# Performance work log

Measured on AMD Instinct MI355X. Metric: run time of the kernel, lower is better.

The kernel has to match this reference:

```python
import jax, jax.numpy as jnp
import numpy as np

N = 50000   # nodes
E = 800000  # edges (avg degree 16)
H = 128     # hidden_dim / emb_dim
OUT = 128   # out_dim
NUM_BOND_TYPE = 6
NUM_BOND_DIR = 6


def setup_inputs() -> dict:
    key = jax.random.key(0)
    ks = jax.random.split(key, 12)
    s = 0.05
    return {
        "x": jax.random.normal(ks[0], (N, H), jnp.float32),
        "edge_index": jax.random.randint(ks[1], (2, E), 0, N),
        "edge_attr": jax.random.randint(ks[2], (E, 2), 0, 6),
        "prelu_a": jnp.float32(0.25),  # PReLU single shared slope (torch default)
        "W_enc": jax.random.normal(ks[3], (H, H), jnp.float32) * s,  # enc_to_dec, no bias
        "edge_emb1": jax.random.normal(ks[4], (NUM_BOND_TYPE, H), jnp.float32) * s,
        "edge_emb2": jax.random.normal(ks[5], (NUM_BOND_DIR, H), jnp.float32) * s,
        "W1": jax.random.normal(ks[6], (H, 2 * H), jnp.float32) * s,
        "b1": jnp.zeros((2 * H,), jnp.float32),
        "W2": jax.random.normal(ks[7], (2 * H, OUT), jnp.float32) * s,
        "b2": jnp.zeros((OUT,), jnp.float32),
    }


def reference(x, edge_index, edge_attr, prelu_a, W_enc, edge_emb1, edge_emb2, W1, b1, W2, b2):
    n = x.shape[0]
    # GNNDecoder: PReLU then enc_to_dec linear (no bias)
    x = jnp.where(x > 0, x, prelu_a * x)
    x = x @ W_enc

    # GINConv.forward: add self loops, self-loop edge_attr = [5, 0]
    loop = jnp.arange(n)
    src = jnp.concatenate([edge_index[0], loop])  # [E+N]
    dst = jnp.concatenate([edge_index[1], loop])  # [E+N]
    ea1 = jnp.concatenate([edge_attr[:, 0], jnp.full((n,), 5, edge_attr.dtype)])
    ea2 = jnp.concatenate([edge_attr[:, 1], jnp.zeros((n,), edge_attr.dtype)])

    # edge embedding lookup + gather-add message + scatter-add aggregate
    edge_emb = edge_emb1[ea1] + edge_emb2[ea2]          # [E+N, H]
    msg = x[src] + edge_emb                             # message(x_j, edge_attr)
    agg = jax.ops.segment_sum(msg, dst, num_segments=n)  # aggr='add'

    # update: MLP Linear(H,2H) -> SiLU -> Linear(2H,OUT)
    h = jax.nn.silu(agg @ W1 + b1)
    return h @ W2 + b2
```

## Files before the change

### kernel.cpp

```cpp
#include <hip/hip_runtime.h>

typedef unsigned short u16;
typedef unsigned int   u32;
typedef __attribute__((ext_vector_type(8))) short short8;
typedef __attribute__((ext_vector_type(4))) float f32x4;

__device__ __forceinline__ float bl(u32 u){ union{u32 i; float f;} c; c.i = u << 16; return c.f; }
__device__ __forceinline__ float bh(u32 u){ union{u32 i; float f;} c; c.i = u & 0xffff0000u; return c.f; }
__device__ __forceinline__ u16 f2b(float f){
  union{float f; u32 i;} c; c.f = f;
  return (u16)((c.i + 0x8000u) >> 16);
}
__device__ __forceinline__ u32 pk2(float a, float b){
  union{float f; u32 i;} x, y; x.f = a; y.f = b;
  return ((x.i + 0x8000u) >> 16) | ((y.i + 0x8000u) & 0xffff0000u);
}

__device__ __forceinline__ void wave_scan_bsum(
    const int* __restrict__ bsum, int nb, int* __restrict__ sPre, int t)
{
  int carry = 0;
  for (int c0 = 0; c0 < nb; c0 += 64) {
    int idx = c0 + t;
    int b = (idx < nb) ? bsum[idx] : 0;
    int v = b;
    #pragma unroll
    for (int d = 1; d < 64; d <<= 1) {
      int u = __shfl_up(v, d);
      if (t >= d) v += u;
    }
    if (idx < nb) sPre[idx] = carry + v - b;
    carry += __shfl(v, 63);
  }
}

__global__ __launch_bounds__(256) void k_enc_count(
    const float* __restrict__ x, const float* __restrict__ pa,
    const float* __restrict__ Wenc, u16* __restrict__ xencQ, int N,
    const int* __restrict__ ei, int* __restrict__ cnt,
    int* __restrict__ rank, int E, int encBlocks)
{
  if ((int)blockIdx.x >= encBlocks) {
    int e = ((int)blockIdx.x - encBlocks) * 256 + threadIdx.x;
    if (e < E) rank[e] = atomicAdd(&cnt[ei[E + e]], 1);
    return;
  }

  const int SK = 136, NT = 8;
  __shared__ u16 sB[128 * SK];

  const int t = threadIdx.x;
  for (int j = 0; j < 64; j++) {
    int i = t + 256 * j;
    int k = i >> 7, n = i & 127;
    sB[n * SK + k] = f2b(Wenc[i]);
  }
  __syncthreads();

  const float slope = pa[0];
  const int lane = t & 63, wave = t >> 6, quad = lane >> 4, l16 = lane & 15;
  const int m0 = blockIdx.x * 128 + wave * 32;
  if (m0 >= N) return;

  f32x4 acc[2][NT];
  #pragma unroll
  for (int mr = 0; mr < 2; mr++)
    #pragma unroll
    for (int nt = 0; nt < NT; nt++) acc[mr][nt] = (f32x4){0.f, 0.f, 0.f, 0.f};

  #pragma unroll
  for (int ks = 0; ks < 4; ks++) {
    const int k0 = ks * 32 + quad * 8;
    union { u32 u[4]; short8 s; } a[2];
    #pragma unroll
    for (int mr = 0; mr < 2; mr++) {
      int row = m0 + mr * 16 + l16; row = min(row, N - 1);
      const float4* ap = (const float4*)&x[(size_t)row * 128 + k0];
      float4 f0 = ap[0], f1 = ap[1];
      float v0 = f0.x > 0.f ? f0.x : slope * f0.x;
      float v1 = f0.y > 0.f ? f0.y : slope * f0.y;
      float v2 = f0.z > 0.f ? f0.z : slope * f0.z;
      float v3 = f0.w > 0.f ? f0.w : slope * f0.w;
      float v4 = f1.x > 0.f ? f1.x : slope * f1.x;
      float v5 = f1.y > 0.f ? f1.y : slope * f1.y;
      float v6 = f1.z > 0.f ? f1.z : slope * f1.z;
      float v7 = f1.w > 0.f ? f1.w : slope * f1.w;
      a[mr].u[0] = pk2(v0, v1); a[mr].u[1] = pk2(v2, v3);
      a[mr].u[2] = pk2(v4, v5); a[mr].u[3] = pk2(v6, v7);
    }
    #pragma unroll
    for (int nt = 0; nt < NT; nt++) {
      short8 b = *(const short8*)&sB[(nt * 16 + l16) * SK + k0];
      acc[0][nt] = __builtin_amdgcn_mfma_f32_16x16x32_bf16(a[0].s, b, acc[0][nt], 0, 0, 0);
      acc[1][nt] = __builtin_amdgcn_mfma_f32_16x16x32_bf16(a[1].s, b, acc[1][nt], 0, 0, 0);
    }
  }

  #pragma unroll
  for (int mr = 0; mr < 2; mr++)
    #pragma unroll
    for (int nt = 0; nt < NT; nt++) {
      int col = nt * 16 + l16;
      int q = col >> 5, cq = col & 31;
      #pragma unroll
      for (int r = 0; r < 4; r++) {
        int row = m0 + mr * 16 + quad * 4 + r;
        if (row < N)
          xencQ[((size_t)q * N + row) * 32 + cq] = f2b(acc[mr][nt][r]);
      }
    }
}

__global__ __launch_bounds__(256) void k_scanW(
    const int* __restrict__ cnt, int* __restrict__ offs,
    int* __restrict__ bsum, int n, int nb,
    const float* __restrict__ W1, const float* __restrict__ W2,
    const float* __restrict__ e1, const float* __restrict__ e2,
    u16* __restrict__ W1T, u16* __restrict__ W2T, u32* __restrict__ embP)
{
  if ((int)blockIdx.x >= nb) {
    int i = ((int)blockIdx.x - nb) * 256 + threadIdx.x;
    if (i < 32768) {
      int nn = i >> 7, k = i & 127;
      W1T[i] = f2b(W1[k * 256 + nn]);
    } else if (i < 65536) {
      int j = i - 32768;
      int nn = j >> 8, k = j & 255;
      W2T[j] = f2b(W2[k * 128 + nn]);
    } else {
      int j = i - 65536;
      int q = j / 576, rem = j - q * 576;
      int c = rem >> 4, s = rem & 15;
      int c1 = c / 6, c2 = c - c1 * 6;
      int col = q * 32 + s * 2;
      embP[j] = pk2(e1[c1 * 128 + col]     + e2[c2 * 128 + col],
                    e1[c1 * 128 + col + 1] + e2[c2 * 128 + col + 1]);
    }
    return;
  }

  __shared__ int sS[256];
  const int b = blockIdx.x, t = threadIdx.x;
  const int i0 = b * 1024 + t * 4;
  int4 v = make_int4(0, 0, 0, 0);
  if (i0 + 3 < n) v = *(const int4*)&cnt[i0];
  else {
    if (i0     < n) v.x = cnt[i0];
    if (i0 + 1 < n) v.y = cnt[i0 + 1];
    if (i0 + 2 < n) v.z = cnt[i0 + 2];
  }
  int s = v.x + v.y + v.z + v.w;
  sS[t] = s;
  __syncthreads();
  for (int d = 1; d < 256; d <<= 1) {
    int val = (t >= d) ? sS[t - d] : 0;
    __syncthreads();
    sS[t] += val;
    __syncthreads();
  }
  int ex = sS[t] - s;
  if (t == 255) bsum[b] = sS[t];
  int o0 = ex, o1 = o0 + v.x, o2 = o1 + v.y, o3 = o2 + v.z;
  if (i0     < n) offs[i0]     = o0;
  if (i0 + 1 < n) offs[i0 + 1] = o1;
  if (i0 + 2 < n) offs[i0 + 2] = o2;
  if (i0 + 3 < n) offs[i0 + 3] = o3;
}

__global__ __launch_bounds__(256) void k_fill(
    const int* __restrict__ ei, const int* __restrict__ ea,
    const int* __restrict__ offs, const int* __restrict__ rank,
    const int* __restrict__ bsum, int nb,
    u32* __restrict__ recs, int E)
{
  __shared__ int sPre[256];
  const int t = threadIdx.x;
  if (t < 64) wave_scan_bsum(bsum, nb, sPre, t);
  __syncthreads();

  int e = blockIdx.x * 256 + t;
  if (e >= E) return;
  int src = ei[e];
  int dst = ei[E + e];
  int2 a = *(const int2*)&ea[2 * e];
  int pos = offs[dst] + sPre[dst >> 10] + rank[e];
  recs[pos] = (u32)src | ((u32)(a.x * 6 + a.y) << 26);
}

struct B8 { uint2 x[8]; u32 r[8]; };

__device__ __forceinline__ void issue8(B8& b, u32 rv, int grp,
                                       const u32* __restrict__ xq, int sub) {
  #pragma unroll
  for (int k = 0; k < 8; k++) {
    u32 r = __shfl(rv, grp + k);
    b.r[k] = r;
    b.x[k] = *(const uint2*)&xq[(size_t)(r & 0x3ffffffu) * 16 + sub * 2];
  }
}

__device__ __forceinline__ void acc8(float* a, const B8& b,
                                     const u32* __restrict__ sEq,
                                     int sub, int dleft) {
  #pragma unroll
  for (int k = 0; k < 8; k++) {
    if (k < dleft) {
      uint2 e = *(const uint2*)&sEq[(b.r[k] >> 26) * 18 + sub * 2];
      uint2 x = b.x[k];
      a[0] += bl(x.x) + bl(e.x);  a[1] += bh(x.x) + bh(e.x);
      a[2] += bl(x.y) + bl(e.y);  a[3] += bh(x.y) + bh(e.y);
    }
  }
}

__global__ __launch_bounds__(256, 4) void k_gather(
    const int* __restrict__ offs, const int* __restrict__ bsum, int nb,
    const u32* __restrict__ recs, const u32* __restrict__ embP,
    const u32* __restrict__ xencQ, u32* __restrict__ aggbQ, int N, int E)
{
  const int ES = 18;
  __shared__ u32 sE[4 * 36 * ES];
  __shared__ int sPre[256];

  const int t = threadIdx.x;
  for (int i = t; i < 4 * 36 * 16; i += 256) {
    int qc = i >> 4, s = i & 15;
    sE[qc * ES + s] = embP[i];
  }
  if (t < 64) wave_scan_bsum(bsum, nb, sPre, t);
  __syncthreads();

  const int lane = t & 63, wave = t >> 6;
  const int grp = lane & 56, sub = lane & 7;
  const int v = blockIdx.x * 32 + wave * 8 + (lane >> 3);
  const bool vok = v < N;
  const int vc = vok ? v : N - 1;
  const int beg = offs[vc] + sPre[vc >> 10];
  const int end = (vc == N - 1) ? E : (offs[vc + 1] + sPre[(vc + 1) >> 10]);
  const int d = vok ? end - beg : 0;

  u32 rv0 = 0, rv1 = 0, rv2 = 0, rv3 = 0;
  if (d > 0)  rv0 = recs[min(beg + sub, end - 1)];
  if (d > 8)  rv1 = recs[min(beg + 8 + sub, end - 1)];
  if (d > 16) rv2 = recs[min(beg + 16 + sub, end - 1)];
  if (d > 24) rv3 = recs[min(beg + 24 + sub, end - 1)];

  #pragma unroll 1
  for (int q = 0; q < 4; q++) {
    const u32* xq = xencQ + (size_t)q * N * 16;
    const u32* sEq = &sE[q * 36 * ES];

    uint2 xs = *(const uint2*)&xq[(size_t)vc * 16 + sub * 2];
    uint2 es = *(const uint2*)&sEq[30 * ES + sub * 2];
    float a[4];
    a[0] = bl(xs.x) + bl(es.x);  a[1] = bh(xs.x) + bh(es.x);
    a[2] = bl(xs.y) + bl(es.y);  a[3] = bh(xs.y) + bh(es.y);

    if (d > 0) {
      B8 bA, bB;
      issue8(bA, rv0, grp, xq, sub);
      if (d > 8) issue8(bB, rv1, grp, xq, sub);
      acc8(a, bA, sEq, sub, d);
      if (d > 8) {
        if (d > 16) issue8(bA, rv2, grp, xq, sub);
        acc8(a, bB, sEq, sub, d - 8);
        if (d > 16) {
          if (d > 24) issue8(bB, rv3, grp, xq, sub);
          acc8(a, bA, sEq, sub, d - 16);
          if (d > 24) {
            acc8(a, bB, sEq, sub, d - 24);
            for (int j0 = 32; j0 < d; j0 += 8) {
              u32 rvt = recs[min(beg + j0 + sub, end - 1)];
              issue8(bA, rvt, grp, xq, sub);
              acc8(a, bA, sEq, sub, d - j0);
            }
          }
        }
      }
    }

    if (vok) {
      uint2 o;
      o.x = pk2(a[0], a[1]);
      o.y = pk2(a[2], a[3]);
      *(uint2*)&aggbQ[((size_t)q * N + vc) * 16 + sub * 2] = o;
    }
  }
}

__global__ __launch_bounds__(256) void k_mlp(
    const u16* __restrict__ aggbQ, const u16* __restrict__ W1T,
    const float* __restrict__ b1, const u16* __restrict__ W2T,
    const float* __restrict__ b2, float* __restrict__ out, int N)
{
  const int SK = 136;
  __shared__ u16 sW[128 * SK];
  __shared__ u16 sH[128 * SK];
  __shared__ float sB1[256];
  __shared__ float sB2[128];

  const int t = threadIdx.x;
  const int lane = t & 63, wave = t >> 6, quad = lane >> 4, l16 = lane & 15;
  const int m0 = blockIdx.x * 128 + wave * 32;

  if (t < 128) sB2[t] = b2[t];
  sB1[t] = b1[t];

  union { uint4 q; short8 s; } a[2][4];
  #pragma unroll
  for (int mr = 0; mr < 2; mr++) {
    int row = min(m0 + mr * 16 + l16, N - 1);
    #pragma unroll
    for (int ks = 0; ks < 4; ks++)
      a[mr][ks].q = *(const uint4*)&aggbQ[((size_t)ks * N + row) * 32 + quad * 8];
  }

  f32x4 acc2[2][8];
  #pragma unroll
  for (int mr = 0; mr < 2; mr++)
    #pragma unroll
    for (int nt = 0; nt < 8; nt++) acc2[mr][nt] = (f32x4){0.f, 0.f, 0.f, 0.f};

  for (int half = 0; half < 2; half++) {
    #pragma unroll
    for (int j = 0; j < 8; j++) {
      int i = t + 256 * j;
      int n = i >> 4, k8 = i & 15;
      *(uint4*)&sW[n * SK + k8 * 8] =
          *(const uint4*)&W1T[(size_t)(half * 128 + n) * 128 + k8 * 8];
    }
    __syncthreads();

    f32x4 acc1[2][8];
    #pragma unroll
    for (int mr = 0; mr < 2; mr++)
      #pragma unroll
      for (int nt = 0; nt < 8; nt++) acc1[mr][nt] = (f32x4){0.f, 0.f, 0.f, 0.f};

    #pragma unroll
    for (int ks = 0; ks < 4; ks++) {
      const int k0 = ks * 32 + quad * 8;
      #pragma unroll
      for (int nt = 0; nt < 8; nt++) {
        short8 b = *(const short8*)&sW[(nt * 16 + l16) * SK + k0];
        acc1[0][nt] = __builtin_amdgcn_mfma_f32_16x16x32_bf16(a[0][ks].s, b, acc1[0][nt], 0, 0, 0);
        acc1[1][nt] = __builtin_amdgcn_mfma_f32_16x16x32_bf16(a[1][ks].s, b, acc1[1][nt], 0, 0, 0);
      }
    }

    #pragma unroll
    for (int mr = 0; mr < 2; mr++)
      #pragma unroll
      for (int nt = 0; nt < 8; nt++) {
        int col = nt * 16 + l16;
        float bias = sB1[half * 128 + col];
        #pragma unroll
        for (int r = 0; r < 4; r++) {
          float z = acc1[mr][nt][r] + bias;
          float s = z / (1.f + __expf(-z));
          sH[(wave * 32 + mr * 16 + quad * 4 + r) * SK + col] = f2b(s);
        }
      }
    __syncthreads();

    #pragma unroll
    for (int j = 0; j < 8; j++) {
      int i = t + 256 * j;
      int n = i >> 4, k8 = i & 15;
      *(uint4*)&sW[n * SK + k8 * 8] =
          *(const uint4*)&W2T[(size_t)n * 256 + half * 128 + k8 * 8];
    }
    __syncthreads();

    #pragma unroll
    for (int ks = 0; ks < 4; ks++) {
      const int k0 = ks * 32 + quad * 8;
      union { uint4 q; short8 s; } ah[2];
      #pragma unroll
      for (int mr = 0; mr < 2; mr++)
        ah[mr].q = *(const uint4*)&sH[(wave * 32 + mr * 16 + l16) * SK + k0];
      #pragma unroll
      for (int nt = 0; nt < 8; nt++) {
        short8 b = *(const short8*)&sW[(nt * 16 + l16) * SK + k0];
        acc2[0][nt] = __builtin_amdgcn_mfma_f32_16x16x32_bf16(ah[0].s, b, acc2[0][nt], 0, 0, 0);
        acc2[1][nt] = __builtin_amdgcn_mfma_f32_16x16x32_bf16(ah[1].s, b, acc2[1][nt], 0, 0, 0);
      }
    }
    __syncthreads();
  }

  #pragma unroll
  for (int mr = 0; mr < 2; mr++)
    #pragma unroll
    for (int nt = 0; nt < 8; nt++) {
      int col = nt * 16 + l16;
      float bias = sB2[col];
      #pragma unroll
      for (int r = 0; r < 4; r++) {
        int row = m0 + mr * 16 + quad * 4 + r;
        if (row < N) out[(size_t)row * 128 + col] = acc2[mr][nt][r] + bias;
      }
    }
}

extern "C" void kernel_launch(void* const* d_in, const int* in_sizes, int n_in,
                              void* d_out, int out_size, void* d_ws, size_t ws_size,
                              hipStream_t stream) {
  const float* x    = (const float*)d_in[0];
  const int*   ei   = (const int*)d_in[1];
  const int*   ea   = (const int*)d_in[2];
  const float* pa   = (const float*)d_in[3];
  const float* Wenc = (const float*)d_in[4];
  const float* e1   = (const float*)d_in[5];
  const float* e2   = (const float*)d_in[6];
  const float* W1   = (const float*)d_in[7];
  const float* b1   = (const float*)d_in[8];
  const float* W2   = (const float*)d_in[9];
  const float* b2   = (const float*)d_in[10];
  float* out = (float*)d_out;

  const int N = in_sizes[0] / 128;
  const int E = in_sizes[1] / 2;

  char* ws = (char*)d_ws;
  size_t off = 0;
  auto alloc = [&](size_t bytes) {
    void* p = ws + off;
    off = (off + bytes + 255) & ~(size_t)255;
    return p;
  };
  u16*   xencQ  = (u16*)  alloc((size_t)N * 128 * 2);
  u32*   aggbQ  = (u32*)  alloc((size_t)N * 64 * 4);
  int*   cnt    = (int*)  alloc((size_t)N * 4);
  int*   offs   = (int*)  alloc((size_t)(N + 1) * 4);
  int*   rank   = (int*)  alloc((size_t)E * 4);
  int*   bsum   = (int*)  alloc(256 * 4);
  u32*   recs   = (u32*)  alloc((size_t)(E + 64) * 4);
  u16*   W1T    = (u16*)  alloc(256 * 128 * 2);
  u16*   W2T    = (u16*)  alloc(128 * 256 * 2);
  u32*   embP   = (u32*)  alloc(2304 * 4);

  const int encBlocks    = (N + 127) / 128;
  const int edgeBlocks   = (E + 255) / 256;
  const int nb           = (N + 1023) / 1024;
  const int gatherBlocks = (N + 31) / 32;

  hipMemsetAsync(cnt, 0, (size_t)N * 4, stream);
  k_enc_count<<<encBlocks + edgeBlocks, 256, 0, stream>>>(
      x, pa, Wenc, xencQ, N, ei, cnt, rank, E, encBlocks);
  k_scanW<<<nb + 265, 256, 0, stream>>>(
      cnt, offs, bsum, N, nb, W1, W2, e1, e2, W1T, W2T, embP);
  k_fill<<<edgeBlocks, 256, 0, stream>>>(ei, ea, offs, rank, bsum, nb, recs, E);
  k_gather<<<gatherBlocks, 256, 0, stream>>>(
      offs, bsum, nb, recs, embP, (const u32*)xencQ, aggbQ, N, E);
  k_mlp<<<encBlocks, 256, 0, stream>>>(
      (const u16*)aggbQ, W1T, b1, W2T, b2, out, N);
}
```

Before: 224.0 us.

## Split gather across quarter-column blocks and pre-transpose Wenc in a prep kernel

The gather kernel no longer loops over the four 32-column quarters inside one block. The quarter index now comes from the block index, so the grid is four times larger, each block holds a quarter of the embedding table in LDS, and the occupancy hint on launch bounds is removed. A new prep kernel transposes Wenc to bf16, builds the packed edge-embedding table, and zeroes the degree counters, replacing the memset. Each encoder block then loads the pre-converted weights with vector loads instead of converting 64 floats per thread. The trade-off is an extra launch, plus the CSR offsets and records being read four times across the gather blocks.

```diff
diff --git a/kernel.cpp b/kernel.cpp
--- a/kernel.cpp
+++ b/kernel.cpp
@@ -34,9 +34,32 @@
   }
 }
 
+__global__ __launch_bounds__(256) void k_pre(
+    const float* __restrict__ Wenc, const float* __restrict__ e1,
+    const float* __restrict__ e2, u16* __restrict__ WencT,
+    u32* __restrict__ embP, int* __restrict__ cnt, int N)
+{
+  int i = blockIdx.x * 256 + threadIdx.x;
+  if (i < 16384) {
+    int n = i >> 7, k = i & 127;
+    WencT[i] = f2b(Wenc[k * 128 + n]);
+  } else if (i < 16384 + 2304) {
+    int j = i - 16384;
+    int q = j / 576, rem = j - q * 576;
+    int c = rem >> 4, s = rem & 15;
+    int c1 = c / 6, c2 = c - c1 * 6;
+    int col = q * 32 + s * 2;
+    embP[j] = pk2(e1[c1 * 128 + col]     + e2[c2 * 128 + col],
+                  e1[c1 * 128 + col + 1] + e2[c2 * 128 + col + 1]);
+  } else {
+    int j = i - 16384 - 2304;
+    if (j < N) cnt[j] = 0;
+  }
+}
+
 __global__ __launch_bounds__(256) void k_enc_count(
     const float* __restrict__ x, const float* __restrict__ pa,
-    const float* __restrict__ Wenc, u16* __restrict__ xencQ, int N,
+    const u16* __restrict__ WT, u16* __restrict__ xencQ, int N,
     const int* __restrict__ ei, int* __restrict__ cnt,
     int* __restrict__ rank, int E, int encBlocks)
 {
@@ -50,10 +73,11 @@
   __shared__ u16 sB[128 * SK];
 
   const int t = threadIdx.x;
-  for (int j = 0; j < 64; j++) {
+  #pragma unroll
+  for (int j = 0; j < 8; j++) {
     int i = t + 256 * j;
-    int k = i >> 7, n = i & 127;
-    sB[n * SK + k] = f2b(Wenc[i]);
+    int n = i >> 4, k8 = i & 15;
+    *(uint4*)&sB[n * SK + k8 * 8] = *(const uint4*)&WT[n * 128 + k8 * 8];
   }
   __syncthreads();
 
@@ -115,26 +139,17 @@
     const int* __restrict__ cnt, int* __restrict__ offs,
     int* __restrict__ bsum, int n, int nb,
     const float* __restrict__ W1, const float* __restrict__ W2,
-    const float* __restrict__ e1, const float* __restrict__ e2,
-    u16* __restrict__ W1T, u16* __restrict__ W2T, u32* __restrict__ embP)
+    u16* __restrict__ W1T, u16* __restrict__ W2T)
 {
   if ((int)blockIdx.x >= nb) {
     int i = ((int)blockIdx.x - nb) * 256 + threadIdx.x;
     if (i < 32768) {
       int nn = i >> 7, k = i & 127;
       W1T[i] = f2b(W1[k * 256 + nn]);
-    } else if (i < 65536) {
+    } else {
       int j = i - 32768;
       int nn = j >> 8, k = j & 255;
       W2T[j] = f2b(W2[k * 128 + nn]);
-    } else {
-      int j = i - 65536;
-      int q = j / 576, rem = j - q * 576;
-      int c = rem >> 4, s = rem & 15;
-      int c1 = c / 6, c2 = c - c1 * 6;
-      int col = q * 32 + s * 2;
-      embP[j] = pk2(e1[c1 * 128 + col]     + e2[c2 * 128 + col],
-                    e1[c1 * 128 + col + 1] + e2[c2 * 128 + col + 1]);
     }
     return;
   }
@@ -213,26 +228,30 @@
   }
 }
 
-__global__ __launch_bounds__(256, 4) void k_gather(
+__global__ __launch_bounds__(256) void k_gather(
     const int* __restrict__ offs, const int* __restrict__ bsum, int nb,
     const u32* __restrict__ recs, const u32* __restrict__ embP,
-    const u32* __restrict__ xencQ, u32* __restrict__ aggbQ, int N, int E)
+    const u32* __restrict__ xencQ, u32* __restrict__ aggbQ,
+    int N, int E, int nodeBlocks)
 {
   const int ES = 18;
-  __shared__ u32 sE[4 * 36 * ES];
+  __shared__ u32 sE[36 * ES];
   __shared__ int sPre[256];
 
   const int t = threadIdx.x;
-  for (int i = t; i < 4 * 36 * 16; i += 256) {
-    int qc = i >> 4, s = i & 15;
-    sE[qc * ES + s] = embP[i];
+  const int q = (int)blockIdx.x / nodeBlocks;
+  const int nbid = (int)blockIdx.x - q * nodeBlocks;
+
+  for (int i = t; i < 576; i += 256) {
+    int c = i >> 4, s = i & 15;
+    sE[c * ES + s] = embP[q * 576 + i];
   }
   if (t < 64) wave_scan_bsum(bsum, nb, sPre, t);
   __syncthreads();
 
   const int lane = t & 63, wave = t >> 6;
   const int grp = lane & 56, sub = lane & 7;
-  const int v = blockIdx.x * 32 + wave * 8 + (lane >> 3);
+  const int v = nbid * 32 + wave * 8 + (lane >> 3);
   const bool vok = v < N;
   const int vc = vok ? v : N - 1;
   const int beg = offs[vc] + sPre[vc >> 10];
@@ -245,46 +264,42 @@
   if (d > 16) rv2 = recs[min(beg + 16 + sub, end - 1)];
   if (d > 24) rv3 = recs[min(beg + 24 + sub, end - 1)];
 
-  #pragma unroll 1
-  for (int q = 0; q < 4; q++) {
-    const u32* xq = xencQ + (size_t)q * N * 16;
-    const u32* sEq = &sE[q * 36 * ES];
-
-    uint2 xs = *(const uint2*)&xq[(size_t)vc * 16 + sub * 2];
-    uint2 es = *(const uint2*)&sEq[30 * ES + sub * 2];
-    float a[4];
-    a[0] = bl(xs.x) + bl(es.x);  a[1] = bh(xs.x) + bh(es.x);
-    a[2] = bl(xs.y) + bl(es.y);  a[3] = bh(xs.y) + bh(es.y);
-
-    if (d > 0) {
-      B8 bA, bB;
-      issue8(bA, rv0, grp, xq, sub);
-      if (d > 8) issue8(bB, rv1, grp, xq, sub);
-      acc8(a, bA, sEq, sub, d);
-      if (d > 8) {
-        if (d > 16) issue8(bA, rv2, grp, xq, sub);
-        acc8(a, bB, sEq, sub, d - 8);
-        if (d > 16) {
-          if (d > 24) issue8(bB, rv3, grp, xq, sub);
-          acc8(a, bA, sEq, sub, d - 16);
-          if (d > 24) {
-            acc8(a, bB, sEq, sub, d - 24);
-            for (int j0 = 32; j0 < d; j0 += 8) {
-              u32 rvt = recs[min(beg + j0 + sub, end - 1)];
-              issue8(bA, rvt, grp, xq, sub);
-              acc8(a, bA, sEq, sub, d - j0);
-            }
+  const u32* xq = xencQ + (size_t)q * N * 16;
+
+  uint2 xs = *(const uint2*)&xq[(size_t)vc * 16 + sub * 2];
+  uint2 es = *(const uint2*)&sE[30 * ES + sub * 2];
+  float a[4];
+  a[0] = bl(xs.x) + bl(es.x);  a[1] = bh(xs.x) + bh(es.x);
+  a[2] = bl(xs.y) + bl(es.y);  a[3] = bh(xs.y) + bh(es.y);
+
+  if (d > 0) {
+    B8 bA, bB;
+    issue8(bA, rv0, grp, xq, sub);
+    if (d > 8) issue8(bB, rv1, grp, xq, sub);
+    acc8(a, bA, sE, sub, d);
+    if (d > 8) {
+      if (d > 16) issue8(bA, rv2, grp, xq, sub);
+      acc8(a, bB, sE, sub, d - 8);
+      if (d > 16) {
+        if (d > 24) issue8(bB, rv3, grp, xq, sub);
+        acc8(a, bA, sE, sub, d - 16);
+        if (d > 24) {
+          acc8(a, bB, sE, sub, d - 24);
+          for (int j0 = 32; j0 < d; j0 += 8) {
+            u32 rvt = recs[min(beg + j0 + sub, end - 1)];
+            issue8(bA, rvt, grp, xq, sub);
+            acc8(a, bA, sE, sub, d - j0);
           }
         }
       }
     }
-
-    if (vok) {
-      uint2 o;
-      o.x = pk2(a[0], a[1]);
-      o.y = pk2(a[2], a[3]);
-      *(uint2*)&aggbQ[((size_t)q * N + vc) * 16 + sub * 2] = o;
-    }
+  }
+
+  if (vok) {
+    uint2 o;
+    o.x = pk2(a[0], a[1]);
+    o.y = pk2(a[2], a[3]);
+    *(uint2*)&aggbQ[((size_t)q * N + vc) * 16 + sub * 2] = o;
   }
 }
 
@@ -436,6 +451,7 @@
   int*   rank   = (int*)  alloc((size_t)E * 4);
   int*   bsum   = (int*)  alloc(256 * 4);
   u32*   recs   = (u32*)  alloc((size_t)(E + 64) * 4);
+  u16*   WencT  = (u16*)  alloc(128 * 128 * 2);
   u16*   W1T    = (u16*)  alloc(256 * 128 * 2);
   u16*   W2T    = (u16*)  alloc(128 * 256 * 2);
   u32*   embP   = (u32*)  alloc(2304 * 4);
@@ -443,16 +459,17 @@
   const int encBlocks    = (N + 127) / 128;
   const int edgeBlocks   = (E + 255) / 256;
   const int nb           = (N + 1023) / 1024;
-  const int gatherBlocks = (N + 31) / 32;
-
-  hipMemsetAsync(cnt, 0, (size_t)N * 4, stream);
+  const int nodeBlocks   = (N + 31) / 32;
+  const int preBlocks    = (16384 + 2304 + N + 255) / 256;
+
+  k_pre<<<preBlocks, 256, 0, stream>>>(Wenc, e1, e2, WencT, embP, cnt, N);
   k_enc_count<<<encBlocks + edgeBlocks, 256, 0, stream>>>(
-      x, pa, Wenc, xencQ, N, ei, cnt, rank, E, encBlocks);
-  k_scanW<<<nb + 265, 256, 0, stream>>>(
-      cnt, offs, bsum, N, nb, W1, W2, e1, e2, W1T, W2T, embP);
+      x, pa, WencT, xencQ, N, ei, cnt, rank, E, encBlocks);
+  k_scanW<<<nb + 256, 256, 0, stream>>>(
+      cnt, offs, bsum, N, nb, W1, W2, W1T, W2T);
   k_fill<<<edgeBlocks, 256, 0, stream>>>(ei, ea, offs, rank, bsum, nb, recs, E);
-  k_gather<<<gatherBlocks, 256, 0, stream>>>(
-      offs, bsum, nb, recs, embP, (const u32*)xencQ, aggbQ, N, E);
+  k_gather<<<4 * nodeBlocks, 256, 0, stream>>>(
+      offs, bsum, nb, recs, embP, (const u32*)xencQ, aggbQ, N, E, nodeBlocks);
   k_mlp<<<encBlocks, 256, 0, stream>>>(
       (const u16*)aggbQ, W1T, b1, W2T, b2, out, N);
 }
```

After: 214.6 us. 1.04x faster.
